# Optimization experiments

Hardware: AMD Instinct MI355X
Metric: run time of the kernel (lower is better)

The kernel has to match this reference:

```python
import jax, jax.numpy as jnp
import numpy as np

N = 33554432
MARGIN = 1.0


def setup_inputs() -> dict:
    key = jax.random.key(0)
    k1, k2 = jax.random.split(key)
    predictions = jax.random.normal(k1, (N,), dtype=jnp.float32)
    # labels in {-1, +1}
    labels = 2 * jax.random.randint(k2, (N,), 0, 2, dtype=jnp.int32) - 1
    return {"predictions": predictions, "labels": labels}


def reference(predictions, labels):
    # Original loop math:
    #   over positives: a += 1; b += 2*(margin - p_i); c += (margin - p_i)^2
    #   over negatives: loss += a*p_j^2 + b*p_j + c
    # Vectorized as masked reductions.
    dt = predictions.dtype
    pos = labels == 1
    neg = labels == -1
    z = jnp.where(pos, MARGIN - predictions, jnp.zeros((), dt))  # margin - p on positives
    a = jnp.sum(pos.astype(dt))
    b = 2.0 * jnp.sum(z)
    c = jnp.sum(z * z)
    pn = jnp.where(neg, predictions, jnp.zeros((), dt))
    n_neg = jnp.sum(neg.astype(dt))
    loss = a * jnp.sum(pn * pn) + b * jnp.sum(pn) + c * n_neg
    return loss
```

## Files before the change

### kernel.cpp

```cpp
#include <hip/hip_runtime.h>


constexpr float MARGIN = 1.0f;

#define BANK_STRIDE 32

__device__ __forceinline__ float wave_reduce(float v) {
    #pragma unroll
    for (int off = 32; off > 0; off >>= 1) v += __shfl_down(v, off, 64);
    return v;
}

__global__ __launch_bounds__(256) void hinge2_reduce(
    const float* __restrict__ pred, const int* __restrict__ lab,
    float* __restrict__ ws, int nvec, int nbanks, int bank_stride)
{
    const float4* p4 = reinterpret_cast<const float4*>(pred);
    const int4*   l4 = reinterpret_cast<const int4*>(lab);

    float a = 0.f, sz = 0.f, sz2 = 0.f, sp = 0.f, sp2 = 0.f;

    int idx    = blockIdx.x * blockDim.x + threadIdx.x;
    int stride = gridDim.x * blockDim.x;

    #define ACC(px, lx) do {                         \
        float ispos = ((lx) == 1) ? 1.0f : 0.0f;     \
        float z  = ispos * (MARGIN - (px));          \
        a   += ispos;                                \
        sz  += z;                                    \
        sz2 += z * z;                                \
        float pn = (px) - ispos * (px);              \
        sp  += pn;                                   \
        sp2 += pn * pn;                              \
    } while (0)

    int i = idx;
    for (; i + 3 * stride < nvec; i += 4 * stride) {
        float4 p0 = p4[i];
        float4 p1 = p4[i + stride];
        float4 p2 = p4[i + 2 * stride];
        float4 p3 = p4[i + 3 * stride];
        int4   l0 = l4[i];
        int4   l1 = l4[i + stride];
        int4   l2 = l4[i + 2 * stride];
        int4   l3 = l4[i + 3 * stride];
        ACC(p0.x, l0.x); ACC(p0.y, l0.y); ACC(p0.z, l0.z); ACC(p0.w, l0.w);
        ACC(p1.x, l1.x); ACC(p1.y, l1.y); ACC(p1.z, l1.z); ACC(p1.w, l1.w);
        ACC(p2.x, l2.x); ACC(p2.y, l2.y); ACC(p2.z, l2.z); ACC(p2.w, l2.w);
        ACC(p3.x, l3.x); ACC(p3.y, l3.y); ACC(p3.z, l3.z); ACC(p3.w, l3.w);
    }
    for (; i < nvec; i += stride) {
        float4 p = p4[i];
        int4   l = l4[i];
        ACC(p.x, l.x); ACC(p.y, l.y); ACC(p.z, l.z); ACC(p.w, l.w);
    }
    #undef ACC

    a   = wave_reduce(a);
    sz  = wave_reduce(sz);
    sz2 = wave_reduce(sz2);
    sp  = wave_reduce(sp);
    sp2 = wave_reduce(sp2);

    __shared__ float sdata[4][5];
    int lane = threadIdx.x & 63;
    int wid  = threadIdx.x >> 6;
    if (lane == 0) {
        sdata[wid][0] = a;
        sdata[wid][1] = sz;
        sdata[wid][2] = sz2;
        sdata[wid][3] = sp;
        sdata[wid][4] = sp2;
    }
    __syncthreads();

    if (threadIdx.x == 0) {
        float t0 = 0.f, t1 = 0.f, t2 = 0.f, t3 = 0.f, t4 = 0.f;
        #pragma unroll
        for (int w = 0; w < 4; ++w) {
            t0 += sdata[w][0];
            t1 += sdata[w][1];
            t2 += sdata[w][2];
            t3 += sdata[w][3];
            t4 += sdata[w][4];
        }
        float* bank = ws + (blockIdx.x & (nbanks - 1)) * bank_stride;
        atomicAdd(&bank[0], t0);
        atomicAdd(&bank[1], t1);
        atomicAdd(&bank[2], t2);
        atomicAdd(&bank[3], t3);
        atomicAdd(&bank[4], t4);
    }
}

__global__ __launch_bounds__(256) void hinge2_final(
    const float* __restrict__ ws,
    const float* __restrict__ pred, const int* __restrict__ lab,
    float* __restrict__ out, int n, int tail_start,
    int nbanks, int bank_stride)
{
    int t = threadIdx.x;
    float a = 0.f, sz = 0.f, sz2 = 0.f, sp = 0.f, sp2 = 0.f;
    for (int b = t; b < nbanks; b += 256) {
        const float* bank = ws + b * bank_stride;
        a   += bank[0];
        sz  += bank[1];
        sz2 += bank[2];
        sp  += bank[3];
        sp2 += bank[4];
    }
    a   = wave_reduce(a);
    sz  = wave_reduce(sz);
    sz2 = wave_reduce(sz2);
    sp  = wave_reduce(sp);
    sp2 = wave_reduce(sp2);

    __shared__ float sdata[4][5];
    int lane = t & 63, wid = t >> 6;
    if (lane == 0) {
        sdata[wid][0] = a;  sdata[wid][1] = sz; sdata[wid][2] = sz2;
        sdata[wid][3] = sp; sdata[wid][4] = sp2;
    }
    __syncthreads();

    if (t == 0) {
        double A = 0, SZ = 0, SZ2 = 0, SP = 0, SP2 = 0;
        #pragma unroll
        for (int w = 0; w < 4; ++w) {
            A   += sdata[w][0];
            SZ  += sdata[w][1];
            SZ2 += sdata[w][2];
            SP  += sdata[w][3];
            SP2 += sdata[w][4];
        }
        for (int i = tail_start; i < n; ++i) {
            float p = pred[i];
            if (lab[i] == 1) {
                double z = (double)MARGIN - (double)p;
                A += 1.0; SZ += z; SZ2 += z * z;
            } else {
                SP += (double)p; SP2 += (double)p * (double)p;
            }
        }
        double loss = A * SP2 + 2.0 * SZ * SP + SZ2 * ((double)n - A);
        out[0] = (float)loss;
    }
}

extern "C" void kernel_launch(void* const* d_in, const int* in_sizes, int n_in,
                              void* d_out, int out_size, void* d_ws, size_t ws_size,
                              hipStream_t stream)
{
    const float* pred = (const float*)d_in[0];
    const int*   lab  = (const int*)d_in[1];
    float*       out  = (float*)d_out;
    float*       ws   = (float*)d_ws;

    int n    = in_sizes[0];
    int nvec = n >> 2;
    int tail = nvec << 2;

    int bank_stride = BANK_STRIDE;
    size_t max_banks = ws_size / (bank_stride * sizeof(float));
    int nbanks = 1;
    if (max_banks == 0) { bank_stride = 5; nbanks = 1; }
    else { while (nbanks * 2 <= (int)max_banks && nbanks < 256) nbanks <<= 1; }

    hipMemsetAsync(ws, 0, (size_t)nbanks * bank_stride * sizeof(float), stream);

    const int block  = 256;
    const int blocks = 2048;
    hinge2_reduce<<<blocks, block, 0, stream>>>(pred, lab, ws, nvec, nbanks, bank_stride);
    hinge2_final<<<1, block, 0, stream>>>(ws, pred, lab, out, n, tail, nbanks, bank_stride);
}
```

Baseline: 285.0 us.

## Replace grid-stride loop with one-shot per-block tiles issuing eight loads per thread

Each block now processes a fixed contiguous chunk of 2048 float4 groups. Every thread issues all eight prediction loads and eight label loads up front before accumulating, and the grid is sized to cover the input exactly. This aims to raise memory-level parallelism and remove loop overhead in the bandwidth-bound reduction. The negative-mask term now uses a select instead of a multiply-subtract. In exchange, the grid is larger, so more blocks perform atomic adds into the bank workspace, and the launch bound requests two blocks per CU.

```diff
diff --git a/kernel.cpp b/kernel.cpp
--- a/kernel.cpp
+++ b/kernel.cpp
@@ -4,6 +4,9 @@
 constexpr float MARGIN = 1.0f;
 
 #define BANK_STRIDE 32
+#define BLOCK 256
+#define GPT 8
+#define GROUPS_PER_BLOCK (BLOCK * GPT)
 
 __device__ __forceinline__ float wave_reduce(float v) {
     #pragma unroll
@@ -11,7 +14,7 @@
     return v;
 }
 
-__global__ __launch_bounds__(256) void hinge2_reduce(
+__global__ __launch_bounds__(BLOCK, 2) void hinge2_reduce(
     const float* __restrict__ pred, const int* __restrict__ lab,
     float* __restrict__ ws, int nvec, int nbanks, int bank_stride)
 {
@@ -20,40 +23,43 @@
 
     float a = 0.f, sz = 0.f, sz2 = 0.f, sp = 0.f, sp2 = 0.f;
 
-    int idx    = blockIdx.x * blockDim.x + threadIdx.x;
-    int stride = gridDim.x * blockDim.x;
-
     #define ACC(px, lx) do {                         \
         float ispos = ((lx) == 1) ? 1.0f : 0.0f;     \
         float z  = ispos * (MARGIN - (px));          \
         a   += ispos;                                \
         sz  += z;                                    \
         sz2 += z * z;                                \
-        float pn = (px) - ispos * (px);              \
+        float pn = ((lx) == 1) ? 0.0f : (px);        \
         sp  += pn;                                   \
         sp2 += pn * pn;                              \
     } while (0)
+    #define ACC4(p, l) do {                          \
+        ACC((p).x, (l).x); ACC((p).y, (l).y);        \
+        ACC((p).z, (l).z); ACC((p).w, (l).w);        \
+    } while (0)
 
-    int i = idx;
-    for (; i + 3 * stride < nvec; i += 4 * stride) {
-        float4 p0 = p4[i];
-        float4 p1 = p4[i + stride];
-        float4 p2 = p4[i + 2 * stride];
-        float4 p3 = p4[i + 3 * stride];
-        int4   l0 = l4[i];
-        int4   l1 = l4[i + stride];
-        int4   l2 = l4[i + 2 * stride];
-        int4   l3 = l4[i + 3 * stride];
-        ACC(p0.x, l0.x); ACC(p0.y, l0.y); ACC(p0.z, l0.z); ACC(p0.w, l0.w);
-        ACC(p1.x, l1.x); ACC(p1.y, l1.y); ACC(p1.z, l1.z); ACC(p1.w, l1.w);
-        ACC(p2.x, l2.x); ACC(p2.y, l2.y); ACC(p2.z, l2.z); ACC(p2.w, l2.w);
-        ACC(p3.x, l3.x); ACC(p3.y, l3.y); ACC(p3.z, l3.z); ACC(p3.w, l3.w);
+    const int base = blockIdx.x * GROUPS_PER_BLOCK + threadIdx.x;
+
+    if (base + (GPT - 1) * BLOCK < nvec) {
+        float4 pv[GPT];
+        int4   lv[GPT];
+        #pragma unroll
+        for (int k = 0; k < GPT; ++k) pv[k] = p4[base + k * BLOCK];
+        #pragma unroll
+        for (int k = 0; k < GPT; ++k) lv[k] = l4[base + k * BLOCK];
+        #pragma unroll
+        for (int k = 0; k < GPT; ++k) ACC4(pv[k], lv[k]);
+    } else {
+        for (int k = 0; k < GPT; ++k) {
+            int i = base + k * BLOCK;
+            if (i < nvec) {
+                float4 p = p4[i];
+                int4   l = l4[i];
+                ACC4(p, l);
+            }
+        }
     }
-    for (; i < nvec; i += stride) {
-        float4 p = p4[i];
-        int4   l = l4[i];
-        ACC(p.x, l.x); ACC(p.y, l.y); ACC(p.z, l.z); ACC(p.w, l.w);
-    }
+    #undef ACC4
     #undef ACC
 
     a   = wave_reduce(a);
@@ -168,8 +174,8 @@
 
     hipMemsetAsync(ws, 0, (size_t)nbanks * bank_stride * sizeof(float), stream);
 
-    const int block  = 256;
-    const int blocks = 2048;
-    hinge2_reduce<<<blocks, block, 0, stream>>>(pred, lab, ws, nvec, nbanks, bank_stride);
-    hinge2_final<<<1, block, 0, stream>>>(ws, pred, lab, out, n, tail, nbanks, bank_stride);
+    int blocks = (nvec + GROUPS_PER_BLOCK - 1) / GROUPS_PER_BLOCK;
+    if (blocks < 1) blocks = 1;
+    hinge2_reduce<<<blocks, BLOCK, 0, stream>>>(pred, lab, ws, nvec, nbanks, bank_stride);
+    hinge2_final<<<1, BLOCK, 0, stream>>>(ws, pred, lab, out, n, tail, nbanks, bank_stride);
 }
```

Result: faster. 276.6 us (-2.9%).
